# Optimization experiments

Hardware: AMD Instinct MI355X
Metric: run time of the kernel (lower is better)

## Reference

```python
import jax, jax.numpy as jnp
import numpy as np
from jax import lax

B, L = 4, 2500
Y = 8922
VOCAB = 50002  # vocab_size + 2
E = 100        # embed_size
F = 50         # num_filter_maps
K = 9          # kernel_size
PAD = K // 2


def setup_inputs() -> dict:
    key = jax.random.key(0)
    ks = jax.random.split(key, 8)
    x = jax.random.randint(ks[0], (B, L), 0, VOCAB)
    target = jax.random.uniform(ks[1], (B, Y), dtype=jnp.float32)
    embed_table = jax.random.normal(ks[2], (VOCAB, E), dtype=jnp.float32) * 0.1
    embed_table = embed_table.at[0].set(0.0)  # padding_idx=0
    conv_w = jax.random.normal(ks[3], (F, E, K), dtype=jnp.float32) * (1.0 / np.sqrt(E * K))
    conv_b = jax.random.normal(ks[4], (F,), dtype=jnp.float32) * 0.01
    U_w = jax.random.normal(ks[5], (Y, F), dtype=jnp.float32) * (1.0 / np.sqrt(F))
    final_w = jax.random.normal(ks[6], (Y, F), dtype=jnp.float32) * (1.0 / np.sqrt(F))
    final_b = jax.random.normal(ks[7], (Y,), dtype=jnp.float32) * 0.01
    return {"x": x, "target": target, "embed_table": embed_table,
            "conv_w": conv_w, "conv_b": conv_b, "U_w": U_w,
            "final_w": final_w, "final_b": final_b}


def reference(x, target, embed_table, conv_w, conv_b, U_w, final_w, final_b):
    # embedding lookup (padding_idx=0 rows are zero); dropout is eval-mode identity
    e = embed_table[x] * (x != 0)[..., None].astype(embed_table.dtype)  # [B, L, E]
    # conv1d over sequence: input NCH [B, E, L], kernel OIH [F, E, K], 'same' padding
    h = lax.conv_general_dilated(e.transpose(0, 2, 1), conv_w, (1,), [(PAD, PAD)],
                                 dimension_numbers=("NCH", "OIH", "NCH"))
    h = jnp.tanh(h + conv_b[None, :, None]).transpose(0, 2, 1)  # [B, L, F]
    # label-wise attention
    scores = jnp.einsum("yf,blf->byl", U_w, h)      # [B, Y, L]
    alpha = jax.nn.softmax(scores, axis=2)            # [B, Y, L]
    m = jnp.einsum("byl,blf->byf", alpha, h)         # [B, Y, F]
    y = jnp.einsum("yf,byf->by", final_w, m) + final_b  # [B, Y]
    # BCE with logits, mean reduction
    loss = jnp.mean(jnp.maximum(y, 0.0) - y * target + jnp.log1p(jnp.exp(-jnp.abs(y))))
    yhat = jax.nn.sigmoid(y)
    return (yhat, loss, alpha)
```

## Files before the change

### kernel.cpp

```cpp
#include <hip/hip_runtime.h>
#include <hip/hip_bf16.h>
#include <math.h>

#define B_ 4
#define L_ 2500
#define Y_ 8922
#define E_ 100
#define F_ 50
#define K_ 9

typedef __attribute__((ext_vector_type(8))) short bfrag8;
typedef __attribute__((ext_vector_type(4))) float ffrag4;

#define WS_CWT_F  0
#define WS_DEN_F  0
#define WS_HB_U16 90000
#define WS_M_F    295000
#define WS_PART_F 2079400
#define NBLK_FINAL 140

__device__ __forceinline__ void atomAddF(float* p, float v) {
    unsafeAtomicAdd(p, v);
}

__global__ __launch_bounds__(256) void k0_cwt(const float* __restrict__ conv_w,
                                              float* __restrict__ cwT) {
    int idx = blockIdx.x * 256 + threadIdx.x;
    if (idx < F_ * E_ * K_) {
        int f = idx / (E_ * K_);
        int r = idx % (E_ * K_);
        int e = r / K_;
        int k = r % K_;
        cwT[f * (E_ * K_) + k * E_ + e] = conv_w[idx];
    }
}

#define LT1 32
__global__ __launch_bounds__(256) void k1_embed_conv(
    const int* __restrict__ x, const float* __restrict__ emb_tab,
    const float* __restrict__ cwT, const float* __restrict__ conv_b,
    unsigned short* __restrict__ hb) {
    __shared__ __align__(16) float smem[(LT1 + 8) * E_];
    int b = blockIdx.y;
    int l0 = blockIdx.x * LT1;
    int tid = threadIdx.x;
    for (int idx = tid; idx < (LT1 + 8) * E_; idx += 256) {
        int r = idx / E_, e = idx % E_;
        int l = l0 + r - 4;
        float v = 0.f;
        if (l >= 0 && l < L_) {
            int tok = x[b * L_ + l];
            if (tok != 0) v = emb_tab[tok * E_ + e];
        }
        smem[idx] = v;
    }
    __syncthreads();
    const float4* s4 = (const float4*)smem;
    const float4* w4 = (const float4*)cwT;
    for (int idx = tid; idx < LT1 * F_; idx += 256) {
        int ll = idx / F_, f = idx % F_;
        int l = l0 + ll;
        if (l >= L_) continue;
        float acc = conv_b[f];
        for (int k = 0; k < K_; ++k) {
            const float4* se = s4 + (ll + k) * (E_ / 4);
            const float4* we = w4 + f * (E_ * K_ / 4) + k * (E_ / 4);
#pragma unroll
            for (int e4 = 0; e4 < E_ / 4; ++e4) {
                float4 a = se[e4];
                float4 w = we[e4];
                acc += a.x * w.x + a.y * w.y + a.z * w.z + a.w * w.w;
            }
        }
        __hip_bfloat16 hv = __float2bfloat16(tanhf(acc));
        hb[(size_t)(b * L_ + l) * F_ + f] = *reinterpret_cast<unsigned short*>(&hv);
    }
}

#define YT 64
#define LT 64
#define NLT ((L_ + LT - 1) / LT)
#define NYB ((Y_ + YT - 1) / YT)
#define HSTR 72
#define CH1 4
#define TPC1 (NLT / CH1)
__global__ __launch_bounds__(256) void k2a_denm(
    const float* __restrict__ Uw, const unsigned short* __restrict__ hb,
    float* __restrict__ mws, float* __restrict__ den) {
    __shared__ unsigned short hlf[64][HSTR];
    __shared__ unsigned short hfl[64][HSTR];
    __shared__ unsigned short psh[4][16][HSTR];

    int b = blockIdx.z;
    int y0 = blockIdx.x * YT;
    int ch = blockIdx.y;
    int tid = threadIdx.x;
    int wv = tid >> 6;
    int lane = tid & 63;
    int col = lane & 15;
    int quad = lane >> 4;
    int ywb = y0 + wv * 16;
    int ym = ywb + col;

    bfrag8 uf[2];
#pragma unroll
    for (int kc = 0; kc < 2; ++kc) {
#pragma unroll
        for (int j = 0; j < 8; ++j) {
            int f = kc * 32 + quad * 8 + j;
            float v = (ym < Y_ && f < F_) ? Uw[(size_t)ym * F_ + f] : 0.f;
            __hip_bfloat16 bv = __float2bfloat16(v);
            uf[kc][j] = *reinterpret_cast<short*>(&bv);
        }
    }

    for (int i = tid; i < 64 * 14; i += 256) {
        int r = i / 14, c = 50 + (i % 14);
        hlf[r][c] = 0;
    }
    for (int i = tid; i < 14 * 64; i += 256) {
        int r = 50 + i / 64, c = i % 64;
        hfl[r][c] = (r == 50) ? (unsigned short)0x3F80 : (unsigned short)0;
    }

    ffrag4 macc[4];
#pragma unroll
    for (int nt = 0; nt < 4; ++nt) macc[nt] = (ffrag4){0.f, 0.f, 0.f, 0.f};

    const unsigned short* hbase = hb + (size_t)b * L_ * F_;

    for (int lt = ch * TPC1; lt < ch * TPC1 + TPC1; ++lt) {
        int l0 = lt * LT;
        __syncthreads();
        const unsigned int* src = (const unsigned int*)(hbase + (size_t)l0 * F_);
        for (int d = tid; d < LT * F_ / 2; d += 256) {
            int r = d / 25, c = d % 25;
            unsigned int v = (l0 + r < L_) ? src[d] : 0u;
            *(unsigned int*)&hlf[r][2 * c] = v;
            hfl[2 * c][r] = (unsigned short)(v & 0xFFFF);
            hfl[2 * c + 1][r] = (unsigned short)(v >> 16);
        }
        __syncthreads();
#pragma unroll
        for (int nt = 0; nt < 4; ++nt) {
            ffrag4 s = (ffrag4){0.f, 0.f, 0.f, 0.f};
#pragma unroll
            for (int kc = 0; kc < 2; ++kc) {
                bfrag8 bf = *(const bfrag8*)&hlf[nt * 16 + col][kc * 32 + quad * 8];
                s = __builtin_amdgcn_mfma_f32_16x16x32_bf16(uf[kc], bf, s, 0, 0, 0);
            }
            int l = l0 + nt * 16 + col;
#pragma unroll
            for (int i = 0; i < 4; ++i) {
                float e = (l < L_) ? __expf(s[i]) : 0.f;
                __hip_bfloat16 be = __float2bfloat16(e);
                psh[wv][quad * 4 + i][nt * 16 + col] = *reinterpret_cast<unsigned short*>(&be);
            }
        }
        __syncthreads();
#pragma unroll
        for (int kc = 0; kc < 2; ++kc) {
            bfrag8 af = *(const bfrag8*)&psh[wv][col][kc * 32 + quad * 8];
#pragma unroll
            for (int nt = 0; nt < 4; ++nt) {
                bfrag8 bf = *(const bfrag8*)&hfl[nt * 16 + col][kc * 32 + quad * 8];
                macc[nt] = __builtin_amdgcn_mfma_f32_16x16x32_bf16(af, bf, macc[nt], 0, 0, 0);
            }
        }
    }

#pragma unroll
    for (int nt = 0; nt < 4; ++nt) {
        int f = nt * 16 + col;
#pragma unroll
        for (int i = 0; i < 4; ++i) {
            int y = ywb + quad * 4 + i;
            if (y < Y_) {
                if (f < F_) {
                    atomAddF(&mws[((size_t)b * Y_ + y) * F_ + f], macc[nt][i]);
                } else if (f == F_) {
                    atomAddF(&den[(size_t)b * Y_ + y], macc[nt][i]);
                }
            }
        }
    }
}

#define CH2 10
#define TPC2 (NLT / CH2)
__global__ __launch_bounds__(256) void k2b_alpha(
    const float* __restrict__ Uw, const unsigned short* __restrict__ hb,
    const float* __restrict__ den, float* __restrict__ alpha) {
    __shared__ unsigned short hlf[64][HSTR];

    int b = blockIdx.z;
    int y0 = blockIdx.x * YT;
    int ch = blockIdx.y;
    int tid = threadIdx.x;
    int wv = tid >> 6;
    int lane = tid & 63;
    int col = lane & 15;
    int quad = lane >> 4;
    int ywb = y0 + wv * 16;
    int ym = ywb + col;

    bfrag8 uf[2];
#pragma unroll
    for (int kc = 0; kc < 2; ++kc) {
#pragma unroll
        for (int j = 0; j < 8; ++j) {
            int f = kc * 32 + quad * 8 + j;
            float v = (ym < Y_ && f < F_) ? Uw[(size_t)ym * F_ + f] : 0.f;
            __hip_bfloat16 bv = __float2bfloat16(v);
            uf[kc][j] = *reinterpret_cast<short*>(&bv);
        }
    }

    float rd[4];
#pragma unroll
    for (int i = 0; i < 4; ++i) {
        int y = ywb + quad * 4 + i;
        rd[i] = (y < Y_) ? 1.0f / den[(size_t)b * Y_ + y] : 0.f;
    }

    for (int i = tid; i < 64 * 14; i += 256) {
        int r = i / 14, c = 50 + (i % 14);
        hlf[r][c] = 0;
    }

    const unsigned short* hbase = hb + (size_t)b * L_ * F_;
    float* aout = alpha + (size_t)b * Y_ * L_;

    for (int lt = ch * TPC2; lt < ch * TPC2 + TPC2; ++lt) {
        int l0 = lt * LT;
        __syncthreads();
        const unsigned int* src = (const unsigned int*)(hbase + (size_t)l0 * F_);
        for (int d = tid; d < LT * F_ / 2; d += 256) {
            int r = d / 25, c = d % 25;
            unsigned int v = (l0 + r < L_) ? src[d] : 0u;
            *(unsigned int*)&hlf[r][2 * c] = v;
        }
        __syncthreads();
#pragma unroll
        for (int nt = 0; nt < 4; ++nt) {
            ffrag4 s = (ffrag4){0.f, 0.f, 0.f, 0.f};
#pragma unroll
            for (int kc = 0; kc < 2; ++kc) {
                bfrag8 bf = *(const bfrag8*)&hlf[nt * 16 + col][kc * 32 + quad * 8];
                s = __builtin_amdgcn_mfma_f32_16x16x32_bf16(uf[kc], bf, s, 0, 0, 0);
            }
            int l = l0 + nt * 16 + col;
            if (l < L_) {
#pragma unroll
                for (int i = 0; i < 4; ++i) {
                    int y = ywb + quad * 4 + i;
                    if (y < Y_) aout[(size_t)y * L_ + l] = __expf(s[i]) * rd[i];
                }
            }
        }
    }
}

__global__ __launch_bounds__(256) void k4_final(
    const float* __restrict__ m, const float* __restrict__ den,
    const float* __restrict__ fw, const float* __restrict__ fb,
    const float* __restrict__ target, float* __restrict__ yhat,
    float* __restrict__ part) {
    int idx = blockIdx.x * 256 + threadIdx.x;
    float term = 0.f;
    if (idx < B_ * Y_) {
        int yy = idx % Y_;
        const float* mr = m + (size_t)idx * F_;
        const float* wr = fw + (size_t)yy * F_;
        float dot = 0.f;
#pragma unroll
        for (int f = 0; f < F_; ++f) dot += mr[f] * wr[f];
        float s = fb[yy] + dot / den[idx];
        yhat[idx] = 1.f / (1.f + __expf(-s));
        float t = target[idx];
        term = fmaxf(s, 0.f) - s * t + log1pf(__expf(-fabsf(s)));
    }
    float v = term;
    for (int off = 32; off > 0; off >>= 1) v += __shfl_down(v, off, 64);
    __shared__ float red[4];
    int lane = threadIdx.x & 63, w = threadIdx.x >> 6;
    if (lane == 0) red[w] = v;
    __syncthreads();
    if (threadIdx.x == 0) part[blockIdx.x] = red[0] + red[1] + red[2] + red[3];
}

__global__ __launch_bounds__(256) void k5_loss(const float* __restrict__ part,
                                               float* __restrict__ loss_out) {
    float v = 0.f;
    for (int i = threadIdx.x; i < NBLK_FINAL; i += 256) v += part[i];
    for (int off = 32; off > 0; off >>= 1) v += __shfl_down(v, off, 64);
    __shared__ float red[4];
    int lane = threadIdx.x & 63, w = threadIdx.x >> 6;
    if (lane == 0) red[w] = v;
    __syncthreads();
    if (threadIdx.x == 0) loss_out[0] = (red[0] + red[1] + red[2] + red[3]) / (float)(B_ * Y_);
}

extern "C" void kernel_launch(void* const* d_in, const int* in_sizes, int n_in,
                              void* d_out, int out_size, void* d_ws, size_t ws_size,
                              hipStream_t stream) {
    const int*   x       = (const int*)d_in[0];
    const float* target  = (const float*)d_in[1];
    const float* emb_tab = (const float*)d_in[2];
    const float* conv_w  = (const float*)d_in[3];
    const float* conv_b  = (const float*)d_in[4];
    const float* U_w     = (const float*)d_in[5];
    const float* final_w = (const float*)d_in[6];
    const float* final_b = (const float*)d_in[7];

    float* out = (float*)d_out;
    float* wsf = (float*)d_ws;
    unsigned short* wsu = (unsigned short*)d_ws;

    float* cwT            = wsf + WS_CWT_F;
    float* den            = wsf + WS_DEN_F;
    unsigned short* hbf   = wsu + WS_HB_U16;
    float* mbuf           = wsf + WS_M_F;
    float* part           = wsf + WS_PART_F;

    float* yhat  = out;
    float* loss  = out + (size_t)B_ * Y_;
    float* alpha = loss + 1;

    k0_cwt<<<(F_ * E_ * K_ + 255) / 256, 256, 0, stream>>>(conv_w, cwT);
    k1_embed_conv<<<dim3((L_ + LT1 - 1) / LT1, B_), 256, 0, stream>>>(x, emb_tab, cwT, conv_b, hbf);
    hipMemsetAsync(den, 0, (size_t)B_ * Y_ * sizeof(float), stream);
    hipMemsetAsync(mbuf, 0, (size_t)B_ * Y_ * F_ * sizeof(float), stream);
    k2a_denm<<<dim3(NYB, CH1, B_), 256, 0, stream>>>(U_w, hbf, mbuf, den);
    k2b_alpha<<<dim3(NYB, CH2, B_), 256, 0, stream>>>(U_w, hbf, den, alpha);
    k4_final<<<NBLK_FINAL, 256, 0, stream>>>(mbuf, den, final_w, final_b, target, yhat, part);
    k5_loss<<<1, 256, 0, stream>>>(part, loss);
}
```

Measured before the change: 850.5 us.

## Replace atomic m/den accumulation with per-chunk partials and stage alpha stores in LDS

```diff
diff --git a/kernel.cpp b/kernel.cpp
--- a/kernel.cpp
+++ b/kernel.cpp
@@ -13,15 +13,13 @@
 typedef __attribute__((ext_vector_type(4))) float ffrag4;
 
 #define WS_CWT_F  0
-#define WS_DEN_F  0
 #define WS_HB_U16 90000
-#define WS_M_F    295000
-#define WS_PART_F 2079400
+#define WS_MP_F   295000
+#define BYF_      (B_ * Y_ * F_)
+#define BY_       (B_ * Y_)
+#define WS_DENP_F (WS_MP_F + 4 * BYF_)
+#define WS_PART_F (WS_DENP_F + 4 * BY_)
 #define NBLK_FINAL 140
-
-__device__ __forceinline__ void atomAddF(float* p, float v) {
-    unsafeAtomicAdd(p, v);
-}
 
 __global__ __launch_bounds__(256) void k0_cwt(const float* __restrict__ conv_w,
                                               float* __restrict__ cwT) {
@@ -86,7 +84,7 @@
 #define TPC1 (NLT / CH1)
 __global__ __launch_bounds__(256) void k2a_denm(
     const float* __restrict__ Uw, const unsigned short* __restrict__ hb,
-    float* __restrict__ mws, float* __restrict__ den) {
+    float* __restrict__ mp, float* __restrict__ denp) {
     __shared__ unsigned short hlf[64][HSTR];
     __shared__ unsigned short hfl[64][HSTR];
     __shared__ unsigned short psh[4][16][HSTR];
@@ -169,6 +167,7 @@
         }
     }
 
+    float* mchunk = mp + (size_t)ch * BYF_;
 #pragma unroll
     for (int nt = 0; nt < 4; ++nt) {
         int f = nt * 16 + col;
@@ -177,9 +176,9 @@
             int y = ywb + quad * 4 + i;
             if (y < Y_) {
                 if (f < F_) {
-                    atomAddF(&mws[((size_t)b * Y_ + y) * F_ + f], macc[nt][i]);
+                    mchunk[((size_t)b * Y_ + y) * F_ + f] = macc[nt][i];
                 } else if (f == F_) {
-                    atomAddF(&den[(size_t)b * Y_ + y], macc[nt][i]);
+                    denp[(size_t)ch * BY_ + b * Y_ + y] = macc[nt][i];
                 }
             }
         }
@@ -190,8 +189,9 @@
 #define TPC2 (NLT / CH2)
 __global__ __launch_bounds__(256) void k2b_alpha(
     const float* __restrict__ Uw, const unsigned short* __restrict__ hb,
-    const float* __restrict__ den, float* __restrict__ alpha) {
+    const float* __restrict__ denp, float* __restrict__ alpha) {
     __shared__ unsigned short hlf[64][HSTR];
+    __shared__ float alf[64][68];
 
     int b = blockIdx.z;
     int y0 = blockIdx.x * YT;
@@ -220,7 +220,14 @@
 #pragma unroll
     for (int i = 0; i < 4; ++i) {
         int y = ywb + quad * 4 + i;
-        rd[i] = (y < Y_) ? 1.0f / den[(size_t)b * Y_ + y] : 0.f;
+        float d = 0.f;
+        if (y < Y_) {
+#pragma unroll
+            for (int c = 0; c < CH1; ++c) d += denp[(size_t)c * BY_ + b * Y_ + y];
+            rd[i] = 1.0f / d;
+        } else {
+            rd[i] = 0.f;
+        }
     }
 
     for (int i = tid; i < 64 * 14; i += 256) {
@@ -250,19 +257,35 @@
                 s = __builtin_amdgcn_mfma_f32_16x16x32_bf16(uf[kc], bf, s, 0, 0, 0);
             }
             int l = l0 + nt * 16 + col;
-            if (l < L_) {
-#pragma unroll
-                for (int i = 0; i < 4; ++i) {
-                    int y = ywb + quad * 4 + i;
-                    if (y < Y_) aout[(size_t)y * L_ + l] = __expf(s[i]) * rd[i];
+#pragma unroll
+            for (int i = 0; i < 4; ++i) {
+                float v = (l < L_) ? __expf(s[i]) * rd[i] : 0.f;
+                alf[wv * 16 + quad * 4 + i][nt * 16 + col] = v;
+            }
+        }
+        __syncthreads();
+        int lrem = L_ - l0;
+        if (lrem >= LT) {
+            for (int i4 = tid; i4 < 64 * 16; i4 += 256) {
+                int r = i4 >> 4, c4 = i4 & 15;
+                int y = y0 + r;
+                if (y < Y_) {
+                    float4 v = *(const float4*)&alf[r][c4 * 4];
+                    *(float4*)&aout[(size_t)y * L_ + l0 + c4 * 4] = v;
                 }
             }
+        } else {
+            for (int i = tid; i < 64 * LT; i += 256) {
+                int r = i >> 6, c = i & 63;
+                int y = y0 + r, l = l0 + c;
+                if (y < Y_ && l < L_) aout[(size_t)y * L_ + l] = alf[r][c];
+            }
         }
     }
 }
 
 __global__ __launch_bounds__(256) void k4_final(
-    const float* __restrict__ m, const float* __restrict__ den,
+    const float* __restrict__ mp, const float* __restrict__ denp,
     const float* __restrict__ fw, const float* __restrict__ fb,
     const float* __restrict__ target, float* __restrict__ yhat,
     float* __restrict__ part) {
@@ -270,12 +293,17 @@
     float term = 0.f;
     if (idx < B_ * Y_) {
         int yy = idx % Y_;
-        const float* mr = m + (size_t)idx * F_;
         const float* wr = fw + (size_t)yy * F_;
         float dot = 0.f;
-#pragma unroll
-        for (int f = 0; f < F_; ++f) dot += mr[f] * wr[f];
-        float s = fb[yy] + dot / den[idx];
+        float den = 0.f;
+#pragma unroll
+        for (int c = 0; c < CH1; ++c) {
+            den += denp[(size_t)c * BY_ + idx];
+            const float* mr = mp + (size_t)c * BYF_ + (size_t)idx * F_;
+#pragma unroll
+            for (int f = 0; f < F_; ++f) dot += mr[f] * wr[f];
+        }
+        float s = fb[yy] + dot / den;
         yhat[idx] = 1.f / (1.f + __expf(-s));
         float t = target[idx];
         term = fmaxf(s, 0.f) - s * t + log1pf(__expf(-fabsf(s)));
@@ -318,9 +346,9 @@
     unsigned short* wsu = (unsigned short*)d_ws;
 
     float* cwT            = wsf + WS_CWT_F;
-    float* den            = wsf + WS_DEN_F;
     unsigned short* hbf   = wsu + WS_HB_U16;
-    float* mbuf           = wsf + WS_M_F;
+    float* mpart          = wsf + WS_MP_F;
+    float* denp           = wsf + WS_DENP_F;
     float* part           = wsf + WS_PART_F;
 
     float* yhat  = out;
@@ -329,10 +357,8 @@
 
     k0_cwt<<<(F_ * E_ * K_ + 255) / 256, 256, 0, stream>>>(conv_w, cwT);
     k1_embed_conv<<<dim3((L_ + LT1 - 1) / LT1, B_), 256, 0, stream>>>(x, emb_tab, cwT, conv_b, hbf);
-    hipMemsetAsync(den, 0, (size_t)B_ * Y_ * sizeof(float), stream);
-    hipMemsetAsync(mbuf, 0, (size_t)B_ * Y_ * F_ * sizeof(float), stream);
-    k2a_denm<<<dim3(NYB, CH1, B_), 256, 0, stream>>>(U_w, hbf, mbuf, den);
-    k2b_alpha<<<dim3(NYB, CH2, B_), 256, 0, stream>>>(U_w, hbf, den, alpha);
-    k4_final<<<NBLK_FINAL, 256, 0, stream>>>(mbuf, den, final_w, final_b, target, yhat, part);
+    k2a_denm<<<dim3(NYB, CH1, B_), 256, 0, stream>>>(U_w, hbf, mpart, denp);
+    k2b_alpha<<<dim3(NYB, CH2, B_), 256, 0, stream>>>(U_w, hbf, denp, alpha);
+    k4_final<<<NBLK_FINAL, 256, 0, stream>>>(mpart, denp, final_w, final_b, target, yhat, part);
     k5_loss<<<1, 256, 0, stream>>>(part, loss);
 }
```

Result: faster. 832.1 us (-2.2%).
